# Kernel optimization log

Measured on AMD Instinct MI355X. Metric: run time of the kernel, lower is better.

## Reference

```python
import jax, jax.numpy as jnp
import numpy as np

B, CIN, COUT, K = 8, 64, 64, 3
H, W = 256, 256
PAD = 1


def setup_inputs() -> dict:
    key = jax.random.key(0)
    k1, k2, k3, k4 = jax.random.split(key, 4)
    x = jax.random.normal(k1, (B, CIN, H, W), dtype=jnp.float32)
    alpha = jax.random.uniform(k2, (B, CIN, 1, 1), dtype=jnp.float32)
    # learned params per init_kwargs (groups=1 -> cin_per_group = CIN)
    weight = jax.random.normal(k3, (1, COUT, CIN, K, K), dtype=jnp.float32) * 0.05
    bias = jax.random.normal(k4, (1, COUT), dtype=jnp.float32) * 0.05
    return {"x": x, "alpha": alpha, "weight": weight, "bias": bias}


def reference(x, alpha, weight, bias):
    # cal_dim='cin': per-sample modulated weights
    # alpha: (B, CIN, 1, 1) -> (B, 1, CIN, 1, 1); weight: (1, COUT, CIN, K, K)
    w = alpha[:, None] * weight  # (B, COUT, CIN, K, K)

    def conv_one(xi, wi):
        # xi: (CIN, H, W), wi: (COUT, CIN, K, K)
        out = jax.lax.conv_general_dilated(
            xi[None], wi,
            window_strides=(1, 1),
            padding=[(PAD, PAD), (PAD, PAD)],
            dimension_numbers=("NCHW", "OIHW", "NCHW"),
        )
        return out[0]  # (COUT, H, W)

    out = jax.vmap(conv_one)(x, w)  # (B, COUT, H, W)
    # bias is repeated per-sample in the torch code -> same bias every sample
    return out + bias[0][None, :, None, None]
```

## Files before the change

kernel.cpp:

```cpp
#include <hip/hip_runtime.h>


typedef __attribute__((ext_vector_type(8))) short short8;
typedef __attribute__((ext_vector_type(4))) float float4v;

#define BB 8
#define CI_N 64
#define CO_N 64
#define HH 256
#define WW 256
#define TW 32
#define TH 8
#define HALO_W 34
#define HALO_H 10
#define HALO_PX (HALO_W * HALO_H)
#define RS 72
#define HI_OFF 32

#define NFRAG (2 * 9 * 2 * 4 * 64 * 8)

__device__ __forceinline__ unsigned f2bf(float v) {
    unsigned u = __float_as_uint(v);
    return (u + 0x7FFFu + ((u >> 16) & 1u)) >> 16;
}

__global__ void prepack_w(const float* __restrict__ w, ushort* __restrict__ wp) {
    int idx = blockIdx.x * 256 + threadIdx.x;
    if (idx >= NFRAG) return;
    int j     = idx & 7;
    int lane  = (idx >> 3) & 63;
    int mt    = (idx >> 9) & 3;
    int plane = (idx >> 11) & 1;
    int rest  = idx >> 12;
    int k     = rest % 9;
    int chunk = rest / 9;
    int co = mt * 16 + (lane & 15);
    int ci = chunk * 32 + (lane >> 4) * 8 + j;
    float v = w[(co * CI_N + ci) * 9 + k];
    unsigned hi = f2bf(v);
    float fhi = __uint_as_float(hi << 16);
    unsigned lo = f2bf(v - fhi);
    wp[idx] = (ushort)(plane ? lo : hi);
}

__global__ __launch_bounds__(512, 4) void conv_mfma(
    const float* __restrict__ x,
    const float* __restrict__ alpha,
    const ushort* __restrict__ wp,
    const float* __restrict__ bias,
    float* __restrict__ out)
{
    __shared__ __align__(16) ushort sx[HALO_PX * RS];

    const int tid    = threadIdx.x;
    const int lane   = tid & 63;
    const int w_id   = tid >> 6;
    const int n_lane = lane & 15;
    const int q      = lane >> 4;

    const int id  = blockIdx.x;
    const int b   = id & 7;
    const int t   = id >> 3;
    const int tx  = t & 7;
    const int ty  = t >> 3;
    const int gx0 = tx * TW;
    const int gy0 = ty * TH;

    const int m_half = w_id >> 2;
    const int n_q    = w_id & 3;

    float4v acc[2][4];
#pragma unroll
    for (int mt = 0; mt < 2; ++mt) {
        float4v bi;
#pragma unroll
        for (int r = 0; r < 4; ++r)
            bi[r] = bias[(m_half * 2 + mt) * 16 + q * 4 + r];
#pragma unroll
        for (int nt = 0; nt < 4; ++nt) acc[mt][nt] = bi;
    }

    const float* xb = x + (size_t)b * CI_N * HH * WW;
    const int vbase = (n_q * 2 * HALO_W + n_lane) * RS + q * 8;

    for (int chunk = 0; chunk < 2; ++chunk) {
        if (chunk) __syncthreads();

#pragma unroll
        for (int p = 0; p < 2; ++p) {
            const int cl = w_id * 4 + p * 2;
            const int ci = chunk * 32 + cl;
            const float a0 = alpha[b * CI_N + ci];
            const float a1 = alpha[b * CI_N + ci + 1];
            const float* xp0 = xb + (size_t)ci * HH * WW;
            const float* xp1 = xp0 + HH * WW;
#pragma unroll
            for (int it = 0; it < 6; ++it) {
                int hp = it * 64 + lane;
                if (hp < HALO_PX) {
                    int hy = hp / HALO_W;
                    int hx = hp - hy * HALO_W;
                    int gy = gy0 - 1 + hy;
                    int gx = gx0 - 1 + hx;
                    bool ok = ((unsigned)gy < HH) & ((unsigned)gx < WW);
                    int gidx = gy * WW + gx;
                    float v0 = ok ? xp0[gidx] * a0 : 0.0f;
                    float v1 = ok ? xp1[gidx] * a1 : 0.0f;
                    unsigned h0 = f2bf(v0);
                    unsigned h1 = f2bf(v1);
                    float f0 = __uint_as_float(h0 << 16);
                    float f1 = __uint_as_float(h1 << 16);
                    unsigned l0 = f2bf(v0 - f0);
                    unsigned l1 = f2bf(v1 - f1);
                    *(unsigned*)&sx[hp * RS + cl]          = h0 | (h1 << 16);
                    *(unsigned*)&sx[hp * RS + HI_OFF + cl] = l0 | (l1 << 16);
                }
            }
        }
        __syncthreads();

#pragma unroll
        for (int k = 0; k < 9; ++k) {
            const int dy = k / 3 - 1;
            const int dx = k % 3 - 1;
            short8 a_hi[2], a_lo[2];
#pragma unroll
            for (int mt = 0; mt < 2; ++mt) {
                int fh = ((chunk * 9 + k) * 2 + 0) * 4 + (m_half * 2 + mt);
                int fl = ((chunk * 9 + k) * 2 + 1) * 4 + (m_half * 2 + mt);
                a_hi[mt] = *(const short8*)(wp + (size_t)(fh * 64 + lane) * 8);
                a_lo[mt] = *(const short8*)(wp + (size_t)(fl * 64 + lane) * 8);
            }
#pragma unroll
            for (int nt_i = 0; nt_i < 4; ++nt_i) {
                const int off = ((nt_i >> 1) + 1 + dy) * HALO_W + 1 + (nt_i & 1) * 16 + dx;
                const ushort* bp = &sx[vbase + off * RS];
                short8 b_hi = *(const short8*)bp;
                short8 b_lo = *(const short8*)(bp + HI_OFF);
                acc[0][nt_i] = __builtin_amdgcn_mfma_f32_16x16x32_bf16(a_hi[0], b_hi, acc[0][nt_i], 0, 0, 0);
                acc[1][nt_i] = __builtin_amdgcn_mfma_f32_16x16x32_bf16(a_hi[1], b_hi, acc[1][nt_i], 0, 0, 0);
                acc[0][nt_i] = __builtin_amdgcn_mfma_f32_16x16x32_bf16(a_lo[0], b_hi, acc[0][nt_i], 0, 0, 0);
                acc[1][nt_i] = __builtin_amdgcn_mfma_f32_16x16x32_bf16(a_lo[1], b_hi, acc[1][nt_i], 0, 0, 0);
                acc[0][nt_i] = __builtin_amdgcn_mfma_f32_16x16x32_bf16(a_hi[0], b_lo, acc[0][nt_i], 0, 0, 0);
                acc[1][nt_i] = __builtin_amdgcn_mfma_f32_16x16x32_bf16(a_hi[1], b_lo, acc[1][nt_i], 0, 0, 0);
            }
        }
    }

#pragma unroll
    for (int mt = 0; mt < 2; ++mt) {
        const int m0 = (m_half * 2 + mt) * 16;
#pragma unroll
        for (int nt_i = 0; nt_i < 4; ++nt_i) {
            const int nt = n_q * 4 + nt_i;
            const int gy = gy0 + (nt >> 1);
            const int gx = gx0 + (nt & 1) * 16 + n_lane;
#pragma unroll
            for (int r = 0; r < 4; ++r) {
                const int co = m0 + q * 4 + r;
                out[(((size_t)b * CO_N + co) * HH + gy) * WW + gx] = acc[mt][nt_i][r];
            }
        }
    }
}

extern "C" void kernel_launch(void* const* d_in, const int* in_sizes, int n_in,
                              void* d_out, int out_size, void* d_ws, size_t ws_size,
                              hipStream_t stream) {
    const float* x     = (const float*)d_in[0];
    const float* alpha = (const float*)d_in[1];
    const float* w     = (const float*)d_in[2];
    const float* bias  = (const float*)d_in[3];
    float* out  = (float*)d_out;
    ushort* wpk = (ushort*)d_ws;

    prepack_w<<<dim3((NFRAG + 255) / 256), dim3(256), 0, stream>>>(w, wpk);

    conv_mfma<<<dim3(2048), dim3(512), 0, stream>>>(x, alpha, wpk, bias, out);
}
```

Baseline: 378.9 us.

## Prefetch second channel chunk into registers during first chunk's MFMA compute

Restructures the two-chunk loop so the global loads for the second 32-channel chunk are issued into registers before computing the first chunk, then written to LDS after a barrier. Halo offsets and bounds masks are precomputed once, and each wave now handles four channels per pass instead of two pairs. This hides global load latency behind MFMA work, at the cost of 24 extra live float registers per thread, which can lower occupancy under the 512x4 launch bounds.

```diff
diff --git a/kernel.cpp b/kernel.cpp
--- a/kernel.cpp
+++ b/kernel.cpp
@@ -9,6 +9,7 @@
 #define CO_N 64
 #define HH 256
 #define WW 256
+#define HW (HH * WW)
 #define TW 32
 #define TH 8
 #define HALO_W 34
@@ -80,72 +81,112 @@
         for (int nt = 0; nt < 4; ++nt) acc[mt][nt] = bi;
     }
 
-    const float* xb = x + (size_t)b * CI_N * HH * WW;
+    const float* xb = x + (size_t)b * CI_N * HW;
     const int vbase = (n_q * 2 * HALO_W + n_lane) * RS + q * 8;
 
-    for (int chunk = 0; chunk < 2; ++chunk) {
-        if (chunk) __syncthreads();
-
-#pragma unroll
-        for (int p = 0; p < 2; ++p) {
-            const int cl = w_id * 4 + p * 2;
-            const int ci = chunk * 32 + cl;
-            const float a0 = alpha[b * CI_N + ci];
-            const float a1 = alpha[b * CI_N + ci + 1];
-            const float* xp0 = xb + (size_t)ci * HH * WW;
-            const float* xp1 = xp0 + HH * WW;
-#pragma unroll
-            for (int it = 0; it < 6; ++it) {
-                int hp = it * 64 + lane;
-                if (hp < HALO_PX) {
-                    int hy = hp / HALO_W;
-                    int hx = hp - hy * HALO_W;
-                    int gy = gy0 - 1 + hy;
-                    int gx = gx0 - 1 + hx;
-                    bool ok = ((unsigned)gy < HH) & ((unsigned)gx < WW);
-                    int gidx = gy * WW + gx;
-                    float v0 = ok ? xp0[gidx] * a0 : 0.0f;
-                    float v1 = ok ? xp1[gidx] * a1 : 0.0f;
-                    unsigned h0 = f2bf(v0);
-                    unsigned h1 = f2bf(v1);
-                    float f0 = __uint_as_float(h0 << 16);
-                    float f1 = __uint_as_float(h1 << 16);
-                    unsigned l0 = f2bf(v0 - f0);
-                    unsigned l1 = f2bf(v1 - f1);
-                    *(unsigned*)&sx[hp * RS + cl]          = h0 | (h1 << 16);
-                    *(unsigned*)&sx[hp * RS + HI_OFF + cl] = l0 | (l1 << 16);
-                }
-            }
-        }
-        __syncthreads();
-
-#pragma unroll
-        for (int k = 0; k < 9; ++k) {
-            const int dy = k / 3 - 1;
-            const int dx = k % 3 - 1;
-            short8 a_hi[2], a_lo[2];
-#pragma unroll
-            for (int mt = 0; mt < 2; ++mt) {
-                int fh = ((chunk * 9 + k) * 2 + 0) * 4 + (m_half * 2 + mt);
-                int fl = ((chunk * 9 + k) * 2 + 1) * 4 + (m_half * 2 + mt);
-                a_hi[mt] = *(const short8*)(wp + (size_t)(fh * 64 + lane) * 8);
-                a_lo[mt] = *(const short8*)(wp + (size_t)(fl * 64 + lane) * 8);
-            }
-#pragma unroll
-            for (int nt_i = 0; nt_i < 4; ++nt_i) {
-                const int off = ((nt_i >> 1) + 1 + dy) * HALO_W + 1 + (nt_i & 1) * 16 + dx;
-                const ushort* bp = &sx[vbase + off * RS];
-                short8 b_hi = *(const short8*)bp;
-                short8 b_lo = *(const short8*)(bp + HI_OFF);
-                acc[0][nt_i] = __builtin_amdgcn_mfma_f32_16x16x32_bf16(a_hi[0], b_hi, acc[0][nt_i], 0, 0, 0);
-                acc[1][nt_i] = __builtin_amdgcn_mfma_f32_16x16x32_bf16(a_hi[1], b_hi, acc[1][nt_i], 0, 0, 0);
-                acc[0][nt_i] = __builtin_amdgcn_mfma_f32_16x16x32_bf16(a_lo[0], b_hi, acc[0][nt_i], 0, 0, 0);
-                acc[1][nt_i] = __builtin_amdgcn_mfma_f32_16x16x32_bf16(a_lo[1], b_hi, acc[1][nt_i], 0, 0, 0);
-                acc[0][nt_i] = __builtin_amdgcn_mfma_f32_16x16x32_bf16(a_hi[0], b_lo, acc[0][nt_i], 0, 0, 0);
-                acc[1][nt_i] = __builtin_amdgcn_mfma_f32_16x16x32_bf16(a_hi[1], b_lo, acc[1][nt_i], 0, 0, 0);
-            }
-        }
-    }
+    int gofs[6];
+    unsigned okm = 0;
+#pragma unroll
+    for (int it = 0; it < 6; ++it) {
+        int hp = it * 64 + lane;
+        int hy = hp / HALO_W;
+        int hx = hp - hy * HALO_W;
+        int gy = gy0 - 1 + hy;
+        int gx = gx0 - 1 + hx;
+        bool ok = (hp < HALO_PX) & ((unsigned)gy < HH) & ((unsigned)gx < WW);
+        gofs[it] = ok ? gy * WW + gx : 0;
+        okm |= (unsigned)ok << it;
+    }
+    const int cl = w_id * 4;
+    float al0[4], al1[4];
+#pragma unroll
+    for (int j = 0; j < 4; ++j) {
+        al0[j] = alpha[b * CI_N + cl + j];
+        al1[j] = alpha[b * CI_N + 32 + cl + j];
+    }
+
+#define STAGE_LOAD(r, cbase)                                             \
+    {                                                                    \
+        _Pragma("unroll")                                                \
+        for (int j = 0; j < 4; ++j) {                                    \
+            const float* xp = xb + (size_t)((cbase) + cl + j) * HW;      \
+            _Pragma("unroll")                                            \
+            for (int it = 0; it < 6; ++it) r[j][it] = xp[gofs[it]];      \
+        }                                                                \
+    }
+
+#define STAGE_WRITE(r, al)                                               \
+    {                                                                    \
+        _Pragma("unroll")                                                \
+        for (int it = 0; it < 6; ++it) {                                 \
+            if (it < 5 || lane < 20) {         \
+                const int hp = it * 64 + lane;                           \
+                const bool ok = (okm >> it) & 1;                         \
+                float v[4];                                              \
+                _Pragma("unroll")                                        \
+                for (int j = 0; j < 4; ++j)                              \
+                    v[j] = ok ? r[j][it] * al[j] : 0.0f;                 \
+                _Pragma("unroll")                                        \
+                for (int p2 = 0; p2 < 2; ++p2) {                         \
+                    unsigned h0 = f2bf(v[2 * p2]);                       \
+                    unsigned h1 = f2bf(v[2 * p2 + 1]);                   \
+                    unsigned l0 = f2bf(v[2 * p2]                         \
+                                       - __uint_as_float(h0 << 16));     \
+                    unsigned l1 = f2bf(v[2 * p2 + 1]                     \
+                                       - __uint_as_float(h1 << 16));     \
+                    *(unsigned*)&sx[hp * RS + cl + 2 * p2] =             \
+                        h0 | (h1 << 16);                                 \
+                    *(unsigned*)&sx[hp * RS + HI_OFF + cl + 2 * p2] =    \
+                        l0 | (l1 << 16);                                 \
+                }                                                        \
+            }                                                            \
+        }                                                                \
+    }
+
+#define COMPUTE(chunk)                                                   \
+    {                                                                    \
+        _Pragma("unroll")                                                \
+        for (int k = 0; k < 9; ++k) {                                    \
+            const int dy = k / 3 - 1;                                    \
+            const int dx = k % 3 - 1;                                    \
+            short8 a_hi[2], a_lo[2];                                     \
+            _Pragma("unroll")                                            \
+            for (int mt = 0; mt < 2; ++mt) {                             \
+                int fh = (((chunk) * 9 + k) * 2 + 0) * 4 + (m_half * 2 + mt); \
+                int fl = (((chunk) * 9 + k) * 2 + 1) * 4 + (m_half * 2 + mt); \
+                a_hi[mt] = *(const short8*)(wp + (size_t)(fh * 64 + lane) * 8); \
+                a_lo[mt] = *(const short8*)(wp + (size_t)(fl * 64 + lane) * 8); \
+            }                                                            \
+            _Pragma("unroll")                                            \
+            for (int nt_i = 0; nt_i < 4; ++nt_i) {                       \
+                const int off = ((nt_i >> 1) + 1 + dy) * HALO_W + 1      \
+                              + (nt_i & 1) * 16 + dx;                    \
+                const ushort* bp = &sx[vbase + off * RS];                \
+                short8 b_hi = *(const short8*)bp;                        \
+                short8 b_lo = *(const short8*)(bp + HI_OFF);             \
+                acc[0][nt_i] = __builtin_amdgcn_mfma_f32_16x16x32_bf16(a_hi[0], b_hi, acc[0][nt_i], 0, 0, 0); \
+                acc[1][nt_i] = __builtin_amdgcn_mfma_f32_16x16x32_bf16(a_hi[1], b_hi, acc[1][nt_i], 0, 0, 0); \
+                acc[0][nt_i] = __builtin_amdgcn_mfma_f32_16x16x32_bf16(a_lo[0], b_hi, acc[0][nt_i], 0, 0, 0); \
+                acc[1][nt_i] = __builtin_amdgcn_mfma_f32_16x16x32_bf16(a_lo[1], b_hi, acc[1][nt_i], 0, 0, 0); \
+                acc[0][nt_i] = __builtin_amdgcn_mfma_f32_16x16x32_bf16(a_hi[0], b_lo, acc[0][nt_i], 0, 0, 0); \
+                acc[1][nt_i] = __builtin_amdgcn_mfma_f32_16x16x32_bf16(a_hi[1], b_lo, acc[1][nt_i], 0, 0, 0); \
+            }                                                            \
+        }                                                                \
+    }
+
+    float r0[4][6], r1[4][6];
+    STAGE_LOAD(r0, 0);
+    STAGE_WRITE(r0, al0);
+    __syncthreads();
+
+    STAGE_LOAD(r1, 32);
+    COMPUTE(0);
+    __syncthreads();
+
+    STAGE_WRITE(r1, al1);
+    __syncthreads();
+
+    COMPUTE(1);
 
 #pragma unroll
     for (int mt = 0; mt < 2; ++mt) {
@@ -162,6 +203,9 @@
             }
         }
     }
+#undef STAGE_LOAD
+#undef STAGE_WRITE
+#undef COMPUTE
 }
 
 extern "C" void kernel_launch(void* const* d_in, const int* in_sizes, int n_in,
```

Result: faster. 334.2 us (-11.8%).
